# Performance work log

Hardware: AMD Instinct MI355X
Metric: run time of the kernel (lower is better)

Reference implementation:

```python
import jax, jax.numpy as jnp
import numpy as np

B, T, D, U = 32, 512, 1024, 1024
EPS = 1e-08


def setup_inputs() -> dict:
    key = jax.random.key(0)
    k1, k2, k3 = jax.random.split(key, 3)
    # scale weights for numerical sanity (glorot/orthogonal-ish magnitudes)
    kernel = jax.random.normal(k1, (D, 4 * U), dtype=jnp.float32) * (1.0 / np.sqrt(D))
    recurrent_kernel = jax.random.normal(k2, (U, 4 * U), dtype=jnp.float32) * (1.0 / np.sqrt(U))
    bias = jnp.zeros((4 * U,), dtype=jnp.float32)
    x = jax.random.normal(k3, (B, T, D), dtype=jnp.float32)
    return {"x": x, "kernel": kernel, "recurrent_kernel": recurrent_kernel, "bias": bias}


def reference(x, kernel, recurrent_kernel, bias):
    """sLSTM (xLSTM Sec 2.2) with sigmoid forget gate + log/exp/max stabilization,
    scanned over the time axis. Returns h of shape (B, T, U)."""
    U_ = bias.shape[0] // 4
    Bsz = x.shape[0]
    # precompute input projections for all timesteps: (T, B, 4U)
    x_proj = jnp.einsum('btd,dg->tbg', x, kernel) + bias

    def step(carry, xp_t):
        h, c, n, m = carry
        proj = xp_t + h @ recurrent_kernel          # (B, 4U)
        i_p, f_p, o_p, z_p = jnp.split(proj, 4, axis=-1)
        log_f = jnp.log(jax.nn.sigmoid(f_p) + EPS)
        m_t = jnp.maximum(m + log_f, i_p)
        i_t = jnp.exp(i_p - m_t)
        f_t = jnp.exp(m + log_f - m_t)
        o_t = jax.nn.sigmoid(o_p)
        z_t = jnp.tanh(z_p)
        c_t = f_t * c + i_t * z_t
        n_t = f_t * n + i_t
        h_t = o_t * (c_t / (n_t + EPS))
        return (h_t, c_t, n_t, m_t), h_t

    zeros = jnp.zeros((Bsz, U_), dtype=x.dtype)
    init = (zeros, zeros, zeros, zeros)
    _, hs = jax.lax.scan(step, init, x_proj)        # hs: (T, B, U)
    return jnp.transpose(hs, (1, 0, 2))             # (B, T, U)
```

## Files before the change

kernel.cpp:

```cpp
#include <hip/hip_runtime.h>

typedef unsigned short u16;
typedef short short8 __attribute__((ext_vector_type(8)));
typedef float f32x4 __attribute__((ext_vector_type(4)));
typedef unsigned int u32x4 __attribute__((ext_vector_type(4)));
typedef unsigned int u32x2 __attribute__((ext_vector_type(2)));

#define Bsz 32
#define Tsz 512
#define Dsz 1024
#define Usz 1024
#define Gsz 4096

#define SENTINEL 0x7FC0u

static __device__ __forceinline__ u16 f2bf(float f) {
    unsigned int u = __float_as_uint(f);
    unsigned int lsb = (u >> 16) & 1u;
    u += 0x7fffu + lsb;
    return (u16)(u >> 16);
}
static __device__ __forceinline__ float bf2f(u16 b) {
    return __uint_as_float(((unsigned int)b) << 16);
}


__global__ __launch_bounds__(256) void pack_a(const float* __restrict__ x, u16* __restrict__ Af) {
    size_t tid = (size_t)blockIdx.x * 256 + threadIdx.x;
    int L = (int)(tid & 63);
    size_t mtkb = tid >> 6;
    int kb = (int)(mtkb & 31);
    int mt = (int)(mtkb >> 5);
    int m  = mt * 16 + (L & 15);
    int d0 = kb * 32 + (L >> 4) * 8;
    const float* src = x + (size_t)m * Dsz + d0;
    short8 v;
#pragma unroll
    for (int j = 0; j < 8; ++j) v[j] = (short)f2bf(src[j]);
    *(short8*)(Af + tid * 8) = v;
}

__global__ __launch_bounds__(256) void pack_b(const float* __restrict__ W, u16* __restrict__ Bf) {
    size_t tid = (size_t)blockIdx.x * 256 + threadIdx.x;
    int L = (int)(tid & 63);
    size_t ntkb = tid >> 6;
    int kb = (int)(ntkb & 31);
    int nt = (int)(ntkb >> 5);
    int n  = nt * 16 + (L & 15);
    int k0 = kb * 32 + (L >> 4) * 8;
    short8 v;
#pragma unroll
    for (int j = 0; j < 8; ++j) v[j] = (short)f2bf(W[(size_t)(k0 + j) * Gsz + n]);
    *(short8*)(Bf + tid * 8) = v;
}

__global__ __launch_bounds__(256) void pack_r(const float* __restrict__ R, u16* __restrict__ Rp,
                                              u16* __restrict__ hbf) {
    size_t tid = (size_t)blockIdx.x * 256 + threadIdx.x;
    if (tid < 131072) {
        int p = (int)((tid >> 14) & 3);
        hbf[tid] = (p == 3) ? (u16)0 : (u16)SENTINEL;
    }
    int L = (int)(tid & 63);
    size_t bkkb = tid >> 6;
    int kb  = (int)(bkkb & 31);
    int blk = (int)(bkkb >> 5);
    int c = L & 15;
    int gate = c >> 2, du = c & 3;
    int g = gate * 1024 + blk * 4 + du;
    int k0 = kb * 32 + (L >> 4) * 8;
    short8 v;
#pragma unroll
    for (int j = 0; j < 8; ++j) v[j] = (short)f2bf(R[(size_t)(k0 + j) * Gsz + g]);
    *(short8*)(Rp + tid * 8) = v;
}

__global__ __launch_bounds__(256) void gemm1(const u16* __restrict__ Af, const u16* __restrict__ Bf,
                                             float* __restrict__ xpf, u16* __restrict__ xph, int xp32) {
    __shared__ u16 smem[16 * 512];
    int bm = blockIdx.x >> 5;
    int bn = blockIdx.x & 31;
    int tid = threadIdx.x;
    int w = tid >> 6, ln = tid & 63;
    int mw = w & 1, nw = w >> 1;

    f32x4 acc[4][4];
#pragma unroll
    for (int i = 0; i < 4; ++i)
#pragma unroll
        for (int j = 0; j < 4; ++j) acc[i][j] = (f32x4){0.f, 0.f, 0.f, 0.f};

    for (int kb = 0; kb < 32; ++kb) {
        short8 tmp[4];
#pragma unroll
        for (int c2 = 0; c2 < 4; ++c2) {
            int chunk = w * 4 + c2;
            const u16* src = (chunk < 8)
                ? Af + (((size_t)(bm * 8 + chunk) * 32 + kb) * 64 + ln) * 8
                : Bf + (((size_t)(bn * 8 + (chunk - 8)) * 32 + kb) * 64 + ln) * 8;
            tmp[c2] = *(const short8*)src;
        }
#pragma unroll
        for (int c2 = 0; c2 < 4; ++c2) {
            int chunk = w * 4 + c2;
            *(short8*)(smem + chunk * 512 + ln * 8) = tmp[c2];
        }
        __syncthreads();
        short8 av[4], bv[4];
#pragma unroll
        for (int i = 0; i < 4; ++i) av[i] = *(const short8*)(smem + (mw * 4 + i) * 512 + ln * 8);
#pragma unroll
        for (int j = 0; j < 4; ++j) bv[j] = *(const short8*)(smem + (8 + nw * 4 + j) * 512 + ln * 8);
#pragma unroll
        for (int i = 0; i < 4; ++i)
#pragma unroll
            for (int j = 0; j < 4; ++j)
                acc[i][j] = __builtin_amdgcn_mfma_f32_16x16x32_bf16(av[i], bv[j], acc[i][j], 0, 0, 0);
        __syncthreads();
    }

    int quad = ln >> 4, c15 = ln & 15;
#pragma unroll
    for (int i = 0; i < 4; ++i) {
        int mt_g = bm * 8 + mw * 4 + i;
#pragma unroll
        for (int j = 0; j < 4; ++j) {
            int g = (bn * 8 + nw * 4 + j) * 16 + c15;
            int p = ((g & 1023) >> 2) * 16 + (g & 3) * 4 + (g >> 10);
#pragma unroll
            for (int r = 0; r < 4; ++r) {
                int row = mt_g * 16 + quad * 4 + r;
                int bb = row >> 9, tt = row & 511;
                size_t o = ((size_t)tt * Bsz + bb) * Gsz + p;
                if (xp32) xpf[o] = acc[i][j][r];
                else      xph[o] = f2bf(acc[i][j][r]);
            }
        }
    }
}

__global__ __launch_bounds__(384) void scan_all(const float* __restrict__ xpf,
                                                const u16* __restrict__ xph, int xp32,
                                                const u16* __restrict__ Rp,
                                                const float* __restrict__ bias,
                                                u16* __restrict__ hbf, float* __restrict__ out) {
    __shared__ u16 lds_r[16384];
    __shared__ f32x4 partial[2][4][64];
    __shared__ float proj[2][16][17];

    int tid = threadIdx.x;
    int blk = blockIdx.x;
    int w = tid >> 6, ln = tid & 63, quad = ln >> 4, c15 = ln & 15;
    int bq = ln >> 2, du = ln & 3;
    int u_g = blk * 4 + du;

    if (tid < 256) {
#pragma unroll
        for (int i = 0; i < 8; ++i)
            *(short8*)(lds_r + tid * 64 + i * 8) = *(const short8*)(Rp + (size_t)blk * 16384 + tid * 64 + i * 8);
    }

    float bi0 = 0.f, bi1 = 0.f, bi2 = 0.f, bi3 = 0.f;
    float cs = 0.f, ns = 0.f, ms = 0.f;
    f32x4 xr4 = (f32x4){0.f, 0.f, 0.f, 0.f};
    u32x2 xr2 = (u32x2){0u, 0u};

    if (w >= 4) {
        int G = w - 4;
        bi0 = bias[u_g]; bi1 = bias[1024 + u_g]; bi2 = bias[2048 + u_g]; bi3 = bias[3072 + u_g];
        size_t o0 = (size_t)(G * 16 + bq) * Gsz + blk * 16 + du * 4;
        if (xp32) xr4 = *(const f32x4*)(xpf + o0);
        else      xr2 = *(const u32x2*)(xph + o0);
    }
    __syncthreads();

    auto phase = [&](int G, int t) {
        if (w < 4) {
            const u16* hbase = hbf + ((size_t)(G * 4 + ((t + 3) & 3)) << 14)
                                   + (size_t)c15 * 1024 + w * 256 + quad * 8;
            short8 av[8];
            for (;;) {
#define LDH(i, OFF) asm volatile("global_load_dwordx4 %0, %1, off offset:" OFF " sc0 sc1" \
                                 : "=v"(av[i]) : "v"(hbase))
                LDH(0, "0");   LDH(1, "64");  LDH(2, "128"); LDH(3, "192");
                LDH(4, "256"); LDH(5, "320"); LDH(6, "384"); LDH(7, "448");
#undef LDH
                asm volatile("s_waitcnt vmcnt(0)" ::: "memory");
                __builtin_amdgcn_sched_barrier(0);
                unsigned bad = 0;
#pragma unroll
                for (int i = 0; i < 8; ++i) {
                    u32x4 xw = __builtin_bit_cast(u32x4, av[i]);
#pragma unroll
                    for (int k = 0; k < 4; ++k) {
                        unsigned m = xw[k] & 0x7F807F80u;
                        bad |= (unsigned)((m >> 16) == 0x7F80u);
                        bad |= (unsigned)((m & 0xFFFFu) == 0x7F80u);
                    }
                }
                if (!__any((int)bad)) break;
                asm volatile("s_sleep 1" ::: "memory");
            }
            __builtin_amdgcn_sched_barrier(0);

            f32x4 a0 = (f32x4){0.f, 0.f, 0.f, 0.f};
            f32x4 a1 = (f32x4){0.f, 0.f, 0.f, 0.f};
#pragma unroll
            for (int kk = 0; kk < 8; kk += 2) {
                short8 b0 = *(const short8*)(lds_r + ((w * 8 + kk) * 64 + ln) * 8);
                short8 b1 = *(const short8*)(lds_r + ((w * 8 + kk + 1) * 64 + ln) * 8);
                a0 = __builtin_amdgcn_mfma_f32_16x16x32_bf16(av[kk], b0, a0, 0, 0, 0);
                a1 = __builtin_amdgcn_mfma_f32_16x16x32_bf16(av[kk + 1], b1, a1, 0, 0, 0);
            }
            partial[G][w][ln] = a0 + a1;
        }
        __syncthreads();
        if (w == 4 + G) {
            f32x4 s = partial[G][0][ln];
            s += partial[G][1][ln];
            s += partial[G][2][ln];
            s += partial[G][3][ln];
#pragma unroll
            for (int r = 0; r < 4; ++r) proj[G][quad * 4 + r][c15] = s[r];
            asm volatile("s_waitcnt lgkmcnt(0)" ::: "memory");
            __builtin_amdgcn_sched_barrier(0);

            asm volatile("s_waitcnt vmcnt(0)" : "+v"(xr4), "+v"(xr2) :: "memory");
            __builtin_amdgcn_sched_barrier(0);
            float xv0, xv1, xv2, xv3;
            if (xp32) { xv0 = xr4[0]; xv1 = xr4[1]; xv2 = xr4[2]; xv3 = xr4[3]; }
            else {
                xv0 = bf2f((u16)(xr2[0] & 0xffffu)); xv1 = bf2f((u16)(xr2[0] >> 16));
                xv2 = bf2f((u16)(xr2[1] & 0xffffu)); xv3 = bf2f((u16)(xr2[1] >> 16));
            }

            float ip  = proj[G][bq][du]      + xv0 + bi0;
            float fp_ = proj[G][bq][4 + du]  + xv1 + bi1;
            float op_ = proj[G][bq][8 + du]  + xv2 + bi2;
            float zp  = proj[G][bq][12 + du] + xv3 + bi3;
            float sf = 1.f / (1.f + __expf(-fp_));
            float lf = __logf(sf + 1e-8f);
            float mn = fmaxf(ms + lf, ip);
            float it = __expf(ip - mn);
            float ft = __expf(ms + lf - mn);
            float ot = 1.f / (1.f + __expf(-op_));
            float zt = tanhf(zp);
            cs = ft * cs + it * zt;
            ns = ft * ns + it;
            ms = mn;
            float h = ot * (cs / (ns + 1e-8f));
            out[(size_t)(G * 16 + bq) * (Tsz * Usz) + (size_t)t * Usz + u_g] = h;

            size_t chunk = (size_t)bq * 1024 + u_g;
            u16* hp = hbf + ((size_t)(G * 4 + (t & 3)) << 14) + chunk;
            u16* sp = hbf + ((size_t)(G * 4 + ((t + 2) & 3)) << 14) + chunk;
            unsigned hv = (unsigned)f2bf(h);
            unsigned sv = SENTINEL;
            asm volatile("global_store_short %0, %1, off sc0 sc1" :: "v"(hp), "v"(hv) : "memory");
            asm volatile("global_store_short %0, %1, off sc0 sc1" :: "v"(sp), "v"(sv) : "memory");
            asm volatile("s_waitcnt vmcnt(0)" ::: "memory");
            __builtin_amdgcn_sched_barrier(0);

            int tn = (t + 1 < Tsz) ? t + 1 : t;
            size_t o = ((size_t)tn * Bsz + (G * 16 + bq)) * Gsz + blk * 16 + du * 4;
            if (xp32) {
                const float* p = xpf + o;
                asm volatile("global_load_dwordx4 %0, %1, off" : "=v"(xr4) : "v"(p));
            } else {
                const u16* p = xph + o;
                asm volatile("global_load_dwordx2 %0, %1, off" : "=v"(xr2) : "v"(p));
            }
        }
    };

    for (int t = 0; t < Tsz; ++t) {
        phase(0, t);
        phase(1, t);
    }
}

extern "C" void kernel_launch(void* const* d_in, const int* in_sizes, int n_in,
                              void* d_out, int out_size, void* d_ws, size_t ws_size,
                              hipStream_t stream) {
    const float* x    = (const float*)d_in[0];
    const float* W    = (const float*)d_in[1];
    const float* R    = (const float*)d_in[2];
    const float* bias = (const float*)d_in[3];
    float* out = (float*)d_out;

    char* ws = (char*)d_ws;
    size_t off = 0;
    u16* Af = (u16*)(ws + off); off += (size_t)16384 * 1024 * 2;
    u16* Bf = (u16*)(ws + off); off += (size_t)1024 * 4096 * 2;
    u16* Rp = (u16*)(ws + off); off += (size_t)1024 * 4096 * 2;
    u16* hbf = (u16*)(ws + off); off += (size_t)1 << 20;
    off += 4096;
    size_t xp_need32 = (size_t)16384 * 4096 * 4;
    int xp32 = (ws_size >= off + xp_need32) ? 1 : 0;
    float* xpf = (float*)(ws + off);
    u16*   xph = (u16*)(ws + off);

    pack_a<<<dim3(8192), dim3(256), 0, stream>>>(x, Af);
    pack_b<<<dim3(2048), dim3(256), 0, stream>>>(W, Bf);
    pack_r<<<dim3(2048), dim3(256), 0, stream>>>(R, Rp, hbf);
    gemm1<<<dim3(4096), dim3(256), 0, stream>>>(Af, Bf, xpf, xph, xp32);

    void* args[] = { (void*)&xpf, (void*)&xph, (void*)&xp32, (void*)&Rp,
                     (void*)&bias, (void*)&hbf, (void*)&out };
    hipLaunchCooperativeKernel((const void*)scan_all, dim3(256), dim3(384), args, 0, stream);
}
```

Measured before the change: 2.472 ms.

## Process both batch groups concurrently per step with per-chunk sentinel polling

Blocks grow from 384 to 640 threads: eight MFMA waves handle both batch groups at the same time, and two gate waves do the elementwise updates, so each timestep needs one barrier instead of two serialized phases. The partial-sum buffer is double-buffered by timestep parity. The spin-wait now re-polls only the h chunks that still hold a sentinel, instead of reloading all eight. The vmcnt wait after the h stores is removed. Risks are higher register and occupancy pressure, and weaker ordering between the h stores and the loads that follow them.

```diff
diff --git a/kernel.cpp b/kernel.cpp
--- a/kernel.cpp
+++ b/kernel.cpp
@@ -22,6 +22,17 @@
 }
 static __device__ __forceinline__ float bf2f(u16 b) {
     return __uint_as_float(((unsigned int)b) << 16);
+}
+static __device__ __forceinline__ unsigned badchunk(short8 v) {
+    u32x4 xw = __builtin_bit_cast(u32x4, v);
+    unsigned bad = 0;
+#pragma unroll
+    for (int k = 0; k < 4; ++k) {
+        unsigned m = xw[k] & 0x7F807F80u;
+        bad |= (unsigned)((m >> 16) == 0x7F80u);
+        bad |= (unsigned)((m & 0xFFFFu) == 0x7F80u);
+    }
+    return bad;
 }
 
 
@@ -139,13 +150,13 @@
     }
 }
 
-__global__ __launch_bounds__(384) void scan_all(const float* __restrict__ xpf,
+__global__ __launch_bounds__(640) void scan_all(const float* __restrict__ xpf,
                                                 const u16* __restrict__ xph, int xp32,
                                                 const u16* __restrict__ Rp,
                                                 const float* __restrict__ bias,
                                                 u16* __restrict__ hbf, float* __restrict__ out) {
     __shared__ u16 lds_r[16384];
-    __shared__ f32x4 partial[2][4][64];
+    __shared__ f32x4 partial[2][2][4][64];
     __shared__ float proj[2][16][17];
 
     int tid = threadIdx.x;
@@ -154,72 +165,78 @@
     int bq = ln >> 2, du = ln & 3;
     int u_g = blk * 4 + du;
 
-    if (tid < 256) {
-#pragma unroll
-        for (int i = 0; i < 8; ++i)
-            *(short8*)(lds_r + tid * 64 + i * 8) = *(const short8*)(Rp + (size_t)blk * 16384 + tid * 64 + i * 8);
-    }
+    for (int c = tid; c < 2048; c += 640)
+        *(short8*)(lds_r + (size_t)c * 8) = *(const short8*)(Rp + (size_t)blk * 16384 + (size_t)c * 8);
 
     float bi0 = 0.f, bi1 = 0.f, bi2 = 0.f, bi3 = 0.f;
     float cs = 0.f, ns = 0.f, ms = 0.f;
     f32x4 xr4 = (f32x4){0.f, 0.f, 0.f, 0.f};
     u32x2 xr2 = (u32x2){0u, 0u};
 
-    if (w >= 4) {
-        int G = w - 4;
+    if (w >= 8) {
+        int Gg = w - 8;
         bi0 = bias[u_g]; bi1 = bias[1024 + u_g]; bi2 = bias[2048 + u_g]; bi3 = bias[3072 + u_g];
-        size_t o0 = (size_t)(G * 16 + bq) * Gsz + blk * 16 + du * 4;
+        size_t o0 = (size_t)(Gg * 16 + bq) * Gsz + blk * 16 + du * 4;
         if (xp32) xr4 = *(const f32x4*)(xpf + o0);
         else      xr2 = *(const u32x2*)(xph + o0);
     }
     __syncthreads();
 
-    auto phase = [&](int G, int t) {
-        if (w < 4) {
+    int G  = (w < 8) ? (w >> 2) : (w - 8);
+    int wg = w & 3;
+
+    for (int t = 0; t < Tsz; ++t) {
+        if (w < 8) {
             const u16* hbase = hbf + ((size_t)(G * 4 + ((t + 3) & 3)) << 14)
-                                   + (size_t)c15 * 1024 + w * 256 + quad * 8;
+                                   + (size_t)c15 * 1024 + wg * 256 + quad * 8;
             short8 av[8];
-            for (;;) {
 #define LDH(i, OFF) asm volatile("global_load_dwordx4 %0, %1, off offset:" OFF " sc0 sc1" \
                                  : "=v"(av[i]) : "v"(hbase))
-                LDH(0, "0");   LDH(1, "64");  LDH(2, "128"); LDH(3, "192");
-                LDH(4, "256"); LDH(5, "320"); LDH(6, "384"); LDH(7, "448");
-#undef LDH
+            LDH(0, "0");   LDH(1, "64");  LDH(2, "128"); LDH(3, "192");
+            LDH(4, "256"); LDH(5, "320"); LDH(6, "384"); LDH(7, "448");
+            asm volatile("s_waitcnt vmcnt(0)" ::: "memory");
+            __builtin_amdgcn_sched_barrier(0);
+            unsigned dirty = 0;
+#pragma unroll
+            for (int i = 0; i < 8; ++i)
+                if (__any((int)badchunk(av[i]))) dirty |= (1u << i);
+            while (dirty) {
+                asm volatile("s_sleep 2" ::: "memory");
+                if (dirty & 0x01u) LDH(0, "0");
+                if (dirty & 0x02u) LDH(1, "64");
+                if (dirty & 0x04u) LDH(2, "128");
+                if (dirty & 0x08u) LDH(3, "192");
+                if (dirty & 0x10u) LDH(4, "256");
+                if (dirty & 0x20u) LDH(5, "320");
+                if (dirty & 0x40u) LDH(6, "384");
+                if (dirty & 0x80u) LDH(7, "448");
                 asm volatile("s_waitcnt vmcnt(0)" ::: "memory");
                 __builtin_amdgcn_sched_barrier(0);
-                unsigned bad = 0;
-#pragma unroll
-                for (int i = 0; i < 8; ++i) {
-                    u32x4 xw = __builtin_bit_cast(u32x4, av[i]);
-#pragma unroll
-                    for (int k = 0; k < 4; ++k) {
-                        unsigned m = xw[k] & 0x7F807F80u;
-                        bad |= (unsigned)((m >> 16) == 0x7F80u);
-                        bad |= (unsigned)((m & 0xFFFFu) == 0x7F80u);
-                    }
-                }
-                if (!__any((int)bad)) break;
-                asm volatile("s_sleep 1" ::: "memory");
-            }
+#pragma unroll
+                for (int i = 0; i < 8; ++i)
+                    if ((dirty & (1u << i)) && !__any((int)badchunk(av[i]))) dirty &= ~(1u << i);
+            }
+#undef LDH
             __builtin_amdgcn_sched_barrier(0);
 
             f32x4 a0 = (f32x4){0.f, 0.f, 0.f, 0.f};
             f32x4 a1 = (f32x4){0.f, 0.f, 0.f, 0.f};
 #pragma unroll
             for (int kk = 0; kk < 8; kk += 2) {
-                short8 b0 = *(const short8*)(lds_r + ((w * 8 + kk) * 64 + ln) * 8);
-                short8 b1 = *(const short8*)(lds_r + ((w * 8 + kk + 1) * 64 + ln) * 8);
+                short8 b0 = *(const short8*)(lds_r + ((wg * 8 + kk) * 64 + ln) * 8);
+                short8 b1 = *(const short8*)(lds_r + ((wg * 8 + kk + 1) * 64 + ln) * 8);
                 a0 = __builtin_amdgcn_mfma_f32_16x16x32_bf16(av[kk], b0, a0, 0, 0, 0);
                 a1 = __builtin_amdgcn_mfma_f32_16x16x32_bf16(av[kk + 1], b1, a1, 0, 0, 0);
             }
-            partial[G][w][ln] = a0 + a1;
+            partial[G][t & 1][wg][ln] = a0 + a1;
         }
         __syncthreads();
-        if (w == 4 + G) {
-            f32x4 s = partial[G][0][ln];
-            s += partial[G][1][ln];
-            s += partial[G][2][ln];
-            s += partial[G][3][ln];
+        if (w >= 8) {
+            int par = t & 1;
+            f32x4 s = partial[G][par][0][ln];
+            s += partial[G][par][1][ln];
+            s += partial[G][par][2][ln];
+            s += partial[G][par][3][ln];
 #pragma unroll
             for (int r = 0; r < 4; ++r) proj[G][quad * 4 + r][c15] = s[r];
             asm volatile("s_waitcnt lgkmcnt(0)" ::: "memory");
@@ -258,8 +275,6 @@
             unsigned sv = SENTINEL;
             asm volatile("global_store_short %0, %1, off sc0 sc1" :: "v"(hp), "v"(hv) : "memory");
             asm volatile("global_store_short %0, %1, off sc0 sc1" :: "v"(sp), "v"(sv) : "memory");
-            asm volatile("s_waitcnt vmcnt(0)" ::: "memory");
-            __builtin_amdgcn_sched_barrier(0);
 
             int tn = (t + 1 < Tsz) ? t + 1 : t;
             size_t o = ((size_t)tn * Bsz + (G * 16 + bq)) * Gsz + blk * 16 + du * 4;
@@ -271,11 +286,6 @@
                 asm volatile("global_load_dwordx2 %0, %1, off" : "=v"(xr2) : "v"(p));
             }
         }
-    };
-
-    for (int t = 0; t < Tsz; ++t) {
-        phase(0, t);
-        phase(1, t);
     }
 }
 
@@ -307,5 +317,5 @@
 
     void* args[] = { (void*)&xpf, (void*)&xph, (void*)&xp32, (void*)&Rp,
                      (void*)&bias, (void*)&hbf, (void*)&out };
-    hipLaunchCooperativeKernel((const void*)scan_all, dim3(256), dim3(384), args, 0, stream);
-}
+    hipLaunchCooperativeKernel((const void*)scan_all, dim3(256), dim3(640), args, 0, stream);
+}
```

Result: slower. 4.496 ms (+81.9%).

## Give each batch group its own wave doing full-K matvec and gate math, no block barriers

Applied to the files above, without the earlier changes.

The recurrent scan block shrinks from six waves to two. Each wave now owns one batch group and does the whole K=1024 MFMA reduction plus the gate nonlinearity itself, so the per-phase __syncthreads and the LDS partial-sum reduction go away. The h loads are split into two halves, with MFMA on the first half overlapping the second half's arrival, and only chunks still holding the sentinel are re-polled. The cost is fewer waves per step, a longer serial MFMA chain per wave, and more VGPRs for the 32 loaded fragments.

```diff
diff --git a/kernel.cpp b/kernel.cpp
--- a/kernel.cpp
+++ b/kernel.cpp
@@ -22,6 +22,17 @@
 }
 static __device__ __forceinline__ float bf2f(u16 b) {
     return __uint_as_float(((unsigned int)b) << 16);
+}
+static __device__ __forceinline__ unsigned badchunk(short8 v) {
+    u32x4 xw = __builtin_bit_cast(u32x4, v);
+    unsigned bad = 0;
+#pragma unroll
+    for (int k = 0; k < 4; ++k) {
+        unsigned m = xw[k] & 0x7F807F80u;
+        bad |= (unsigned)((m >> 16) == 0x7F80u);
+        bad |= (unsigned)((m & 0xFFFFu) == 0x7F80u);
+    }
+    return bad;
 }
 
 
@@ -139,13 +150,12 @@
     }
 }
 
-__global__ __launch_bounds__(384) void scan_all(const float* __restrict__ xpf,
+__global__ __launch_bounds__(128) void scan_all(const float* __restrict__ xpf,
                                                 const u16* __restrict__ xph, int xp32,
                                                 const u16* __restrict__ Rp,
                                                 const float* __restrict__ bias,
                                                 u16* __restrict__ hbf, float* __restrict__ out) {
     __shared__ u16 lds_r[16384];
-    __shared__ f32x4 partial[2][4][64];
     __shared__ float proj[2][16][17];
 
     int tid = threadIdx.x;
@@ -153,129 +163,183 @@
     int w = tid >> 6, ln = tid & 63, quad = ln >> 4, c15 = ln & 15;
     int bq = ln >> 2, du = ln & 3;
     int u_g = blk * 4 + du;
-
-    if (tid < 256) {
-#pragma unroll
-        for (int i = 0; i < 8; ++i)
-            *(short8*)(lds_r + tid * 64 + i * 8) = *(const short8*)(Rp + (size_t)blk * 16384 + tid * 64 + i * 8);
-    }
-
-    float bi0 = 0.f, bi1 = 0.f, bi2 = 0.f, bi3 = 0.f;
+    const int G = w;
+
+    for (int c = tid; c < 2048; c += 128)
+        *(short8*)(lds_r + (size_t)c * 8) = *(const short8*)(Rp + (size_t)blk * 16384 + (size_t)c * 8);
+
+    float bi0 = bias[u_g], bi1 = bias[1024 + u_g], bi2 = bias[2048 + u_g], bi3 = bias[3072 + u_g];
     float cs = 0.f, ns = 0.f, ms = 0.f;
     f32x4 xr4 = (f32x4){0.f, 0.f, 0.f, 0.f};
     u32x2 xr2 = (u32x2){0u, 0u};
-
-    if (w >= 4) {
-        int G = w - 4;
-        bi0 = bias[u_g]; bi1 = bias[1024 + u_g]; bi2 = bias[2048 + u_g]; bi3 = bias[3072 + u_g];
+    {
         size_t o0 = (size_t)(G * 16 + bq) * Gsz + blk * 16 + du * 4;
         if (xp32) xr4 = *(const f32x4*)(xpf + o0);
         else      xr2 = *(const u32x2*)(xph + o0);
     }
     __syncthreads();
 
-    auto phase = [&](int G, int t) {
-        if (w < 4) {
-            const u16* hbase = hbf + ((size_t)(G * 4 + ((t + 3) & 3)) << 14)
-                                   + (size_t)c15 * 1024 + w * 256 + quad * 8;
-            short8 av[8];
-            for (;;) {
-#define LDH(i, OFF) asm volatile("global_load_dwordx4 %0, %1, off offset:" OFF " sc0 sc1" \
-                                 : "=v"(av[i]) : "v"(hbase))
-                LDH(0, "0");   LDH(1, "64");  LDH(2, "128"); LDH(3, "192");
-                LDH(4, "256"); LDH(5, "320"); LDH(6, "384"); LDH(7, "448");
-#undef LDH
+    size_t afrag = (size_t)c15 * 1024 + (size_t)quad * 8;
+
+    for (int t = 0; t < Tsz; ++t) {
+        const u16* hbase = hbf + ((size_t)(G * 4 + ((t + 3) & 3)) << 14) + afrag;
+        short8 av0[16], av1[16];
+#define LDH0(i, OFF) asm volatile("global_load_dwordx4 %0, %1, off offset:" OFF " sc0 sc1" \
+                                  : "=v"(av0[i]) : "v"(hbase))
+#define LDH1(i, OFF) asm volatile("global_load_dwordx4 %0, %1, off offset:" OFF " sc0 sc1" \
+                                  : "=v"(av1[i]) : "v"(hbase))
+        LDH0(0, "0");    LDH0(1, "64");   LDH0(2, "128");  LDH0(3, "192");
+        LDH0(4, "256");  LDH0(5, "320");  LDH0(6, "384");  LDH0(7, "448");
+        LDH0(8, "512");  LDH0(9, "576");  LDH0(10, "640"); LDH0(11, "704");
+        LDH0(12, "768"); LDH0(13, "832"); LDH0(14, "896"); LDH0(15, "960");
+        LDH1(0, "1024"); LDH1(1, "1088"); LDH1(2, "1152"); LDH1(3, "1216");
+        LDH1(4, "1280"); LDH1(5, "1344"); LDH1(6, "1408"); LDH1(7, "1472");
+        LDH1(8, "1536"); LDH1(9, "1600"); LDH1(10, "1664"); LDH1(11, "1728");
+        LDH1(12, "1792"); LDH1(13, "1856"); LDH1(14, "1920"); LDH1(15, "1984");
+        asm volatile("s_waitcnt vmcnt(16)" ::: "memory");
+        __builtin_amdgcn_sched_barrier(0);
+
+        {
+            unsigned d = 0;
+#pragma unroll
+            for (int i = 0; i < 16; ++i)
+                if (__any((int)badchunk(av0[i]))) d |= (1u << i);
+            while (d) {
+                asm volatile("s_sleep 1" ::: "memory");
+                if (d & 0x0001u) LDH0(0, "0");
+                if (d & 0x0002u) LDH0(1, "64");
+                if (d & 0x0004u) LDH0(2, "128");
+                if (d & 0x0008u) LDH0(3, "192");
+                if (d & 0x0010u) LDH0(4, "256");
+                if (d & 0x0020u) LDH0(5, "320");
+                if (d & 0x0040u) LDH0(6, "384");
+                if (d & 0x0080u) LDH0(7, "448");
+                if (d & 0x0100u) LDH0(8, "512");
+                if (d & 0x0200u) LDH0(9, "576");
+                if (d & 0x0400u) LDH0(10, "640");
+                if (d & 0x0800u) LDH0(11, "704");
+                if (d & 0x1000u) LDH0(12, "768");
+                if (d & 0x2000u) LDH0(13, "832");
+                if (d & 0x4000u) LDH0(14, "896");
+                if (d & 0x8000u) LDH0(15, "960");
                 asm volatile("s_waitcnt vmcnt(0)" ::: "memory");
                 __builtin_amdgcn_sched_barrier(0);
-                unsigned bad = 0;
-#pragma unroll
-                for (int i = 0; i < 8; ++i) {
-                    u32x4 xw = __builtin_bit_cast(u32x4, av[i]);
-#pragma unroll
-                    for (int k = 0; k < 4; ++k) {
-                        unsigned m = xw[k] & 0x7F807F80u;
-                        bad |= (unsigned)((m >> 16) == 0x7F80u);
-                        bad |= (unsigned)((m & 0xFFFFu) == 0x7F80u);
-                    }
-                }
-                if (!__any((int)bad)) break;
+#pragma unroll
+                for (int i = 0; i < 16; ++i)
+                    if ((d & (1u << i)) && !__any((int)badchunk(av0[i]))) d &= ~(1u << i);
+            }
+        }
+        __builtin_amdgcn_sched_barrier(0);
+
+        f32x4 a0 = (f32x4){0.f, 0.f, 0.f, 0.f};
+        f32x4 a1 = (f32x4){0.f, 0.f, 0.f, 0.f};
+#pragma unroll
+        for (int kk = 0; kk < 16; kk += 2) {
+            short8 b0 = *(const short8*)(lds_r + ((kk) * 64 + ln) * 8);
+            short8 b1 = *(const short8*)(lds_r + ((kk + 1) * 64 + ln) * 8);
+            a0 = __builtin_amdgcn_mfma_f32_16x16x32_bf16(av0[kk],     b0, a0, 0, 0, 0);
+            a1 = __builtin_amdgcn_mfma_f32_16x16x32_bf16(av0[kk + 1], b1, a1, 0, 0, 0);
+        }
+
+        asm volatile("s_waitcnt vmcnt(0)" ::: "memory");
+        __builtin_amdgcn_sched_barrier(0);
+        {
+            unsigned d = 0;
+#pragma unroll
+            for (int i = 0; i < 16; ++i)
+                if (__any((int)badchunk(av1[i]))) d |= (1u << i);
+            while (d) {
                 asm volatile("s_sleep 1" ::: "memory");
+                if (d & 0x0001u) LDH1(0, "1024");
+                if (d & 0x0002u) LDH1(1, "1088");
+                if (d & 0x0004u) LDH1(2, "1152");
+                if (d & 0x0008u) LDH1(3, "1216");
+                if (d & 0x0010u) LDH1(4, "1280");
+                if (d & 0x0020u) LDH1(5, "1344");
+                if (d & 0x0040u) LDH1(6, "1408");
+                if (d & 0x0080u) LDH1(7, "1472");
+                if (d & 0x0100u) LDH1(8, "1536");
+                if (d & 0x0200u) LDH1(9, "1600");
+                if (d & 0x0400u) LDH1(10, "1664");
+                if (d & 0x0800u) LDH1(11, "1728");
+                if (d & 0x1000u) LDH1(12, "1792");
+                if (d & 0x2000u) LDH1(13, "1856");
+                if (d & 0x4000u) LDH1(14, "1920");
+                if (d & 0x8000u) LDH1(15, "1984");
+                asm volatile("s_waitcnt vmcnt(0)" ::: "memory");
+                __builtin_amdgcn_sched_barrier(0);
+#pragma unroll
+                for (int i = 0; i < 16; ++i)
+                    if ((d & (1u << i)) && !__any((int)badchunk(av1[i]))) d &= ~(1u << i);
             }
-            __builtin_amdgcn_sched_barrier(0);
-
-            f32x4 a0 = (f32x4){0.f, 0.f, 0.f, 0.f};
-            f32x4 a1 = (f32x4){0.f, 0.f, 0.f, 0.f};
-#pragma unroll
-            for (int kk = 0; kk < 8; kk += 2) {
-                short8 b0 = *(const short8*)(lds_r + ((w * 8 + kk) * 64 + ln) * 8);
-                short8 b1 = *(const short8*)(lds_r + ((w * 8 + kk + 1) * 64 + ln) * 8);
-                a0 = __builtin_amdgcn_mfma_f32_16x16x32_bf16(av[kk], b0, a0, 0, 0, 0);
-                a1 = __builtin_amdgcn_mfma_f32_16x16x32_bf16(av[kk + 1], b1, a1, 0, 0, 0);
-            }
-            partial[G][w][ln] = a0 + a1;
-        }
-        __syncthreads();
-        if (w == 4 + G) {
-            f32x4 s = partial[G][0][ln];
-            s += partial[G][1][ln];
-            s += partial[G][2][ln];
-            s += partial[G][3][ln];
-#pragma unroll
-            for (int r = 0; r < 4; ++r) proj[G][quad * 4 + r][c15] = s[r];
-            asm volatile("s_waitcnt lgkmcnt(0)" ::: "memory");
-            __builtin_amdgcn_sched_barrier(0);
-
-            asm volatile("s_waitcnt vmcnt(0)" : "+v"(xr4), "+v"(xr2) :: "memory");
-            __builtin_amdgcn_sched_barrier(0);
-            float xv0, xv1, xv2, xv3;
-            if (xp32) { xv0 = xr4[0]; xv1 = xr4[1]; xv2 = xr4[2]; xv3 = xr4[3]; }
-            else {
-                xv0 = bf2f((u16)(xr2[0] & 0xffffu)); xv1 = bf2f((u16)(xr2[0] >> 16));
-                xv2 = bf2f((u16)(xr2[1] & 0xffffu)); xv3 = bf2f((u16)(xr2[1] >> 16));
-            }
-
-            float ip  = proj[G][bq][du]      + xv0 + bi0;
-            float fp_ = proj[G][bq][4 + du]  + xv1 + bi1;
-            float op_ = proj[G][bq][8 + du]  + xv2 + bi2;
-            float zp  = proj[G][bq][12 + du] + xv3 + bi3;
-            float sf = 1.f / (1.f + __expf(-fp_));
-            float lf = __logf(sf + 1e-8f);
-            float mn = fmaxf(ms + lf, ip);
-            float it = __expf(ip - mn);
-            float ft = __expf(ms + lf - mn);
-            float ot = 1.f / (1.f + __expf(-op_));
-            float zt = tanhf(zp);
-            cs = ft * cs + it * zt;
-            ns = ft * ns + it;
-            ms = mn;
-            float h = ot * (cs / (ns + 1e-8f));
-            out[(size_t)(G * 16 + bq) * (Tsz * Usz) + (size_t)t * Usz + u_g] = h;
-
-            size_t chunk = (size_t)bq * 1024 + u_g;
-            u16* hp = hbf + ((size_t)(G * 4 + (t & 3)) << 14) + chunk;
-            u16* sp = hbf + ((size_t)(G * 4 + ((t + 2) & 3)) << 14) + chunk;
-            unsigned hv = (unsigned)f2bf(h);
-            unsigned sv = SENTINEL;
-            asm volatile("global_store_short %0, %1, off sc0 sc1" :: "v"(hp), "v"(hv) : "memory");
-            asm volatile("global_store_short %0, %1, off sc0 sc1" :: "v"(sp), "v"(sv) : "memory");
-            asm volatile("s_waitcnt vmcnt(0)" ::: "memory");
-            __builtin_amdgcn_sched_barrier(0);
-
-            int tn = (t + 1 < Tsz) ? t + 1 : t;
-            size_t o = ((size_t)tn * Bsz + (G * 16 + bq)) * Gsz + blk * 16 + du * 4;
-            if (xp32) {
-                const float* p = xpf + o;
-                asm volatile("global_load_dwordx4 %0, %1, off" : "=v"(xr4) : "v"(p));
-            } else {
-                const u16* p = xph + o;
-                asm volatile("global_load_dwordx2 %0, %1, off" : "=v"(xr2) : "v"(p));
-            }
-        }
-    };
-
-    for (int t = 0; t < Tsz; ++t) {
-        phase(0, t);
-        phase(1, t);
+        }
+#undef LDH0
+#undef LDH1
+        __builtin_amdgcn_sched_barrier(0);
+
+#pragma unroll
+        for (int kk = 0; kk < 16; kk += 2) {
+            short8 b0 = *(const short8*)(lds_r + ((16 + kk) * 64 + ln) * 8);
+            short8 b1 = *(const short8*)(lds_r + ((16 + kk + 1) * 64 + ln) * 8);
+            a0 = __builtin_amdgcn_mfma_f32_16x16x32_bf16(av1[kk],     b0, a0, 0, 0, 0);
+            a1 = __builtin_amdgcn_mfma_f32_16x16x32_bf16(av1[kk + 1], b1, a1, 0, 0, 0);
+        }
+        f32x4 acc = a0 + a1;
+
+#pragma unroll
+        for (int r = 0; r < 4; ++r) proj[G][quad * 4 + r][c15] = acc[r];
+        asm volatile("s_waitcnt lgkmcnt(0)" ::: "memory");
+        __builtin_amdgcn_sched_barrier(0);
+        float p_i = proj[G][bq][du];
+        float p_f = proj[G][bq][4 + du];
+        float p_o = proj[G][bq][8 + du];
+        float p_z = proj[G][bq][12 + du];
+        asm volatile("s_waitcnt lgkmcnt(0)" ::: "memory");
+        __builtin_amdgcn_sched_barrier(0);
+
+        float xv0, xv1, xv2, xv3;
+        if (xp32) { xv0 = xr4[0]; xv1 = xr4[1]; xv2 = xr4[2]; xv3 = xr4[3]; }
+        else {
+            xv0 = bf2f((u16)(xr2[0] & 0xffffu)); xv1 = bf2f((u16)(xr2[0] >> 16));
+            xv2 = bf2f((u16)(xr2[1] & 0xffffu)); xv3 = bf2f((u16)(xr2[1] >> 16));
+        }
+
+        float ip  = p_i + xv0 + bi0;
+        float fp_ = p_f + xv1 + bi1;
+        float op_ = p_o + xv2 + bi2;
+        float zp  = p_z + xv3 + bi3;
+        float sf = 1.f / (1.f + __expf(-fp_));
+        float lf = __logf(sf + 1e-8f);
+        float mn = fmaxf(ms + lf, ip);
+        float it = __expf(ip - mn);
+        float ft = __expf(ms + lf - mn);
+        float ot = 1.f / (1.f + __expf(-op_));
+        float zt = tanhf(zp);
+        cs = ft * cs + it * zt;
+        ns = ft * ns + it;
+        ms = mn;
+        float h = ot * (cs / (ns + 1e-8f));
+
+        size_t chunk = (size_t)bq * 1024 + u_g;
+        u16* hp = hbf + ((size_t)(G * 4 + (t & 3)) << 14) + chunk;
+        u16* sp = hbf + ((size_t)(G * 4 + ((t + 2) & 3)) << 14) + chunk;
+        unsigned hv = (unsigned)f2bf(h);
+        unsigned sv = SENTINEL;
+        asm volatile("global_store_short %0, %1, off sc0 sc1" :: "v"(hp), "v"(hv) : "memory");
+        asm volatile("global_store_short %0, %1, off sc0 sc1" :: "v"(sp), "v"(sv) : "memory");
+        asm volatile("s_waitcnt vmcnt(0)" ::: "memory");
+        __builtin_amdgcn_sched_barrier(0);
+
+        out[(size_t)(G * 16 + bq) * (Tsz * Usz) + (size_t)t * Usz + u_g] = h;
+        int tn = (t + 1 < Tsz) ? t + 1 : t;
+        size_t o = ((size_t)tn * Bsz + (G * 16 + bq)) * Gsz + blk * 16 + du * 4;
+        if (xp32) {
+            const float* p = xpf + o;
+            asm volatile("global_load_dwordx4 %0, %1, off" : "=v"(xr4) : "v"(p));
+        } else {
+            const u16* p = xph + o;
+            asm volatile("global_load_dwordx2 %0, %1, off" : "=v"(xr2) : "v"(p));
+        }
     }
 }
 
@@ -307,5 +371,5 @@
 
     void* args[] = { (void*)&xpf, (void*)&xph, (void*)&xp32, (void*)&Rp,
                      (void*)&bias, (void*)&hbf, (void*)&out };
-    hipLaunchCooperativeKernel((const void*)scan_all, dim3(256), dim3(384), args, 0, stream);
-}
+    hipLaunchCooperativeKernel((const void*)scan_all, dim3(256), dim3(128), args, 0, stream);
+}
```

Result: slower. 6.142 ms (+148.5%).
